# Optimization experiments

Measured on AMD Instinct MI355X. Metric: run time of the kernel, lower is better.

## Reference

```python
import jax, jax.numpy as jnp
import numpy as np

B, D, LC, LQ = 64, 256, 1024, 128
P_DROP = 0.1


def setup_inputs() -> dict:
    key = jax.random.key(0)
    k1, k2, k3 = jax.random.split(key, 3)
    C = jax.random.normal(k1, (B, D, LC), dtype=jnp.float32)
    Q = jax.random.normal(k2, (B, D, LQ), dtype=jnp.float32)
    # xavier_normal_ on [B, 1, 3D]: std = sqrt(2 / (fan_in + fan_out)) = sqrt(2 / (1 + 3D))
    std = (2.0 / (1.0 + 3.0 * D)) ** 0.5
    W = jax.random.normal(k3, (B, 1, 3 * D), dtype=jnp.float32) * std
    return {"C": C, "Q": Q, "W": W}


def reference(C, Q, W):
    # Trilinear similarity, algebraically decomposed:
    # S[b,i,j] = W . cat([Q[:,:,j], C[:,:,i], Q[:,:,j]*C[:,:,i]])
    wq, wc, wm = jnp.split(W[:, 0, :], 3, axis=1)          # each [B, D]
    sq = jnp.einsum('bd,bdj->bj', wq, Q)                    # [B, LQ]
    sc = jnp.einsum('bd,bdi->bi', wc, C)                    # [B, LC]
    sm = jnp.einsum('bd,bdi,bdj->bij', wm, C, Q)            # [B, LC, LQ]
    S = sm + sc[:, :, None] + sq[:, None, :]                # [B, LC, LQ]

    S_ = jax.nn.softmax(S, axis=2)    # row softmax over question positions
    S__ = jax.nn.softmax(S, axis=1)   # column softmax over context positions

    # A = Q @ S_^T : [B, D, LC]
    A = jnp.einsum('bdj,bij->bdi', Q, S_)
    # Bmat = C @ (S_ @ S__^T)^T : first M = S__^T-contracted C, then with S_
    M = jnp.einsum('bdk,bkj->bdj', C, S__)                  # [B, D, LQ]
    Bmat = jnp.einsum('bdj,bij->bdi', M, S_)                # [B, D, LC]

    out = jnp.concatenate([C, A, C * A, C * Bmat], axis=1)  # [B, 4D, LC]

    # F.dropout(p, training=True) with a fixed key (deterministic reference)
    keep = jax.random.bernoulli(jax.random.key(42), 1.0 - P_DROP, out.shape)
    return jnp.where(keep, out / (1.0 - P_DROP), 0.0)
```

## Files before the change

### kernel.cpp

```cpp
#include <hip/hip_runtime.h>
#include <stdint.h>
#include <stddef.h>

#define NB  64
#define ND  256
#define NLC 1024
#define NLQ 128
#define INVKEEP (1.0f/0.9f)

#define OFF_SQP   0u
#define OFF_U     32768u
#define OFF_V     98304u
#define OFF_COLP  106496u
#define OFF_SBT   237568u
#define OFF_QT    4431872u
#define OFF_SBF   8544256u
#define OFF_M     12738560u
#define OFF_QB    13787136u

typedef float f32x4  __attribute__((ext_vector_type(4)));
typedef short bf16x8 __attribute__((ext_vector_type(8)));

__device__ __forceinline__ uint32_t f2bf(float x) {
  const uint32_t u = __float_as_uint(x);
  return (u + 0x7fffu + ((u >> 16) & 1u)) >> 16;
}
__device__ __forceinline__ uint32_t cvtpk(float lo, float hi) {
  uint32_t r;
  asm("v_cvt_pk_bf16_f32 %0, %1, %2" : "=v"(r) : "v"(lo), "v"(hi));
  return r;
}

__device__ __forceinline__ void tf_round(uint32_t& a, uint32_t& b, const int r) {
  a += b;
  b = (b << r) | (b >> (32 - r));
  b ^= a;
}
__device__ __forceinline__ uint32_t threefry_xor(uint32_t x0, uint32_t x1) {
  const uint32_t ks0 = 0u, ks1 = 42u, ks2 = 0x1BD11BDAu ^ 0u ^ 42u;
  x0 += ks0; x1 += ks1;
  tf_round(x0,x1,13); tf_round(x0,x1,15); tf_round(x0,x1,26); tf_round(x0,x1,6);
  x0 += ks1; x1 += ks2 + 1u;
  tf_round(x0,x1,17); tf_round(x0,x1,29); tf_round(x0,x1,16); tf_round(x0,x1,24);
  x0 += ks2; x1 += ks0 + 2u;
  tf_round(x0,x1,13); tf_round(x0,x1,15); tf_round(x0,x1,26); tf_round(x0,x1,6);
  x0 += ks0; x1 += ks1 + 3u;
  tf_round(x0,x1,17); tf_round(x0,x1,29); tf_round(x0,x1,16); tf_round(x0,x1,24);
  x0 += ks1; x1 += ks2 + 4u;
  tf_round(x0,x1,13); tf_round(x0,x1,15); tf_round(x0,x1,26); tf_round(x0,x1,6);
  x0 += ks2; x1 += ks0 + 5u;
  return x0 ^ x1;
}

__global__ __launch_bounds__(256) void k_prep(const float* __restrict__ Q,
                                              const float* __restrict__ W,
                                              float* __restrict__ ws) {
  __shared__ __align__(16) float Qs[64][129];
  __shared__ float wqS[64], wmS[64], wcS[64];
  __shared__ float red[8][128];
  const int n = blockIdx.x;
  const int b = n >> 2, c = n & 3;
  const int d0 = c * 64;
  const int t = threadIdx.x;
  if (t < 64) {
    wqS[t] = W[(size_t)b*768 + d0 + t];
    wcS[t] = W[(size_t)b*768 + 256 + d0 + t];
    wmS[t] = W[(size_t)b*768 + 512 + d0 + t];
  }
  __syncthreads();
  const float* Qb = Q + (size_t)b*ND*NLQ;
  ushort* QBg = (ushort*)(ws + OFF_QB) + (size_t)b*ND*NLQ;
  const int j4 = t & 31, y = t >> 5;
  float sq4[4] = {0.0f, 0.0f, 0.0f, 0.0f};
  #pragma unroll
  for (int p = 0; p < 8; ++p) {
    const int dk = p*8 + y;
    const float4 qv = *(const float4*)&Qb[(size_t)(d0+dk)*NLQ + j4*4];
    *(float4*)&Qs[dk][j4*4] = qv;
    uint2 pk;
    pk.x = cvtpk(qv.x, qv.y);
    pk.y = cvtpk(qv.z, qv.w);
    *(uint2*)&QBg[(size_t)(d0+dk)*NLQ + j4*4] = pk;
    const float wq = wqS[dk];
    sq4[0] = fmaf(wq, qv.x, sq4[0]);
    sq4[1] = fmaf(wq, qv.y, sq4[1]);
    sq4[2] = fmaf(wq, qv.z, sq4[2]);
    sq4[3] = fmaf(wq, qv.w, sq4[3]);
  }
  #pragma unroll
  for (int e = 0; e < 4; ++e) red[y][j4*4 + e] = sq4[e];
  __syncthreads();
  const int j = t >> 1, dh = (t & 1) * 32;
  uint32_t pk16[16];
  #pragma unroll
  for (int kk = 0; kk < 32; kk += 2) {
    const float q0 = fmaf(wmS[dh+kk],   Qs[dh+kk][j],   wcS[dh+kk]);
    const float q1 = fmaf(wmS[dh+kk+1], Qs[dh+kk+1][j], wcS[dh+kk+1]);
    pk16[kk >> 1] = cvtpk(q0, q1);
  }
  ushort* QTg = (ushort*)(ws + OFF_QT) + (size_t)b*NLQ*ND + (size_t)j*ND + d0 + dh;
  *(uint4*)&QTg[0]  = *(uint4*)&pk16[0];
  *(uint4*)&QTg[8]  = *(uint4*)&pk16[4];
  *(uint4*)&QTg[16] = *(uint4*)&pk16[8];
  *(uint4*)&QTg[24] = *(uint4*)&pk16[12];
  if (t < 128) {
    float s = 0.0f;
    #pragma unroll
    for (int yy = 0; yy < 8; ++yy) s += red[yy][t];
    ws[OFF_SQP + ((size_t)b*4 + c)*128 + t] = s;
  }
}

__global__ __launch_bounds__(256) void k_s(const float* __restrict__ C,
                                           float* __restrict__ ws) {
  __shared__ __align__(16) uint8_t smem[37376];
  float  (*Cs)[129] = (float(*)[129])smem;
  ushort (*Qt)[40]  = (ushort(*)[40])(smem + 16512);
  ushort (*T)[128]  = (ushort(*)[128])smem;
  float*  sqS       = (float*)(smem + 32768);
  float  (*colm)[128] = (float(*)[128])(smem + 33280);
  float  (*cols)[128] = (float(*)[128])(smem + 35328);

  const int n  = blockIdx.x;
  const int rr = n & 7, qq = n >> 3;
  const int it = qq & 7;
  const int b  = (qq >> 3) * 8 + rr;
  const int i0 = it * 128;
  const int t  = threadIdx.x;
  if (t < 128) {
    const float* sp = ws + OFF_SQP + (size_t)b*4*128 + t;
    sqS[t] = sp[0] + sp[128] + sp[256] + sp[384];
  }

  const float*  Cb  = C + (size_t)b*ND*NLC;
  const ushort* QTg = (const ushort*)(ws + OFF_QT) + (size_t)b*NLQ*ND;
  const int l  = t & 63, w = t >> 6;
  const int lm = l & 15, lg = l >> 4;

  f32x4 acc[2][8];
  #pragma unroll
  for (int mg = 0; mg < 2; ++mg)
    #pragma unroll
    for (int nf = 0; nf < 8; ++nf) acc[mg][nf] = (f32x4)0.0f;

  for (int d0 = 0; d0 < ND; d0 += 32) {
    __syncthreads();
    #pragma unroll
    for (int p = 0; p < 4; ++p) {
      const int f  = p*256 + t;
      const int dk = f >> 5, x4 = f & 31;
      *(float4*)&Cs[dk][x4*4] = *(const float4*)&Cb[(size_t)(d0+dk)*NLC + i0 + x4*4];
    }
    #pragma unroll
    for (int p = 0; p < 2; ++p) {
      const int f  = p*256 + t;
      const int jr = f >> 2, k8 = (f & 3)*8;
      *(uint4*)&Qt[jr][k8] = *(const uint4*)&QTg[(size_t)jr*ND + d0 + k8];
    }
    __syncthreads();
    bf16x8 bq[8];
    #pragma unroll
    for (int nf = 0; nf < 8; ++nf)
      bq[nf] = *(const bf16x8*)&Qt[nf*16 + lm][lg*8];
    #pragma unroll
    for (int mg = 0; mg < 2; ++mg) {
      const int i = w*32 + mg*16 + lm;
      union { uint32_t u[4]; bf16x8 v; } ca;
      #pragma unroll
      for (int kk = 0; kk < 4; ++kk)
        ca.u[kk] = cvtpk(Cs[lg*8 + kk*2][i], Cs[lg*8 + kk*2 + 1][i]);
      #pragma unroll
      for (int nf = 0; nf < 8; ++nf)
        acc[mg][nf] = __builtin_amdgcn_mfma_f32_16x16x32_bf16(ca.v, bq[nf], acc[mg][nf], 0, 0, 0);
    }
  }

  float sqv[8];
  #pragma unroll
  for (int nf = 0; nf < 8; ++nf) sqv[nf] = sqS[nf*16 + lm];
  __syncthreads();

  #pragma unroll
  for (int mg = 0; mg < 2; ++mg) {
    #pragma unroll
    for (int r = 0; r < 4; ++r) {
      const int row = w*32 + mg*16 + lg*4 + r;
      float sv[8], e[8];
      #pragma unroll
      for (int nf = 0; nf < 8; ++nf) sv[nf] = acc[mg][nf][r] + sqv[nf];
      float mx = sv[0];
      #pragma unroll
      for (int nf = 1; nf < 8; ++nf) mx = fmaxf(mx, sv[nf]);
      mx = fmaxf(mx, __shfl_xor(mx, 1));
      mx = fmaxf(mx, __shfl_xor(mx, 2));
      mx = fmaxf(mx, __shfl_xor(mx, 4));
      mx = fmaxf(mx, __shfl_xor(mx, 8));
      float sm = 0.0f;
      #pragma unroll
      for (int nf = 0; nf < 8; ++nf) { e[nf] = __expf(sv[nf] - mx); sm += e[nf]; }
      sm += __shfl_xor(sm, 1); sm += __shfl_xor(sm, 2);
      sm += __shfl_xor(sm, 4); sm += __shfl_xor(sm, 8);
      const float ir = 1.0f / sm;
      const int po = ((row & 7) ^ ((row >> 3) & 7)) << 3;
      #pragma unroll
      for (int nf = 0; nf < 8; ++nf)
        T[row][(nf*16 + lm) ^ po] = (ushort)f2bf(e[nf] * ir);
      if (lm == 0) ws[OFF_U + (size_t)b*NLC + i0 + row] = __expf(mx) * sm;
    }
  }

  float cmx[8];
  #pragma unroll
  for (int nf = 0; nf < 8; ++nf) {
    float m2 = -3.0e38f;
    #pragma unroll
    for (int mg = 0; mg < 2; ++mg)
      #pragma unroll
      for (int r = 0; r < 4; ++r)
        m2 = fmaxf(m2, acc[mg][nf][r] + sqv[nf]);
    m2 = fmaxf(m2, __shfl_xor(m2, 16));
    m2 = fmaxf(m2, __shfl_xor(m2, 32));
    cmx[nf] = m2;
  }
  if (lg == 0) {
    #pragma unroll
    for (int nf = 0; nf < 8; ++nf) colm[w][nf*16 + lm] = cmx[nf];
  }
  __syncthreads();
  #pragma unroll
  for (int nf = 0; nf < 8; ++nf) {
    const int j = nf*16 + lm;
    const float cmb = fmaxf(fmaxf(colm[0][j], colm[1][j]),
                            fmaxf(colm[2][j], colm[3][j]));
    float cs = 0.0f;
    #pragma unroll
    for (int mg = 0; mg < 2; ++mg)
      #pragma unroll
      for (int r = 0; r < 4; ++r)
        cs += __expf(acc[mg][nf][r] + sqv[nf] - cmb);
    cs += __shfl_xor(cs, 16);
    cs += __shfl_xor(cs, 32);
    if (lg == 0) cols[w][j] = cs;
  }
  __syncthreads();

  ushort* Sb16 = (ushort*)(ws + OFF_SBF) + ((size_t)b*NLC + (size_t)i0)*NLQ;
  #pragma unroll
  for (int p = 0; p < 8; ++p) {
    const int f = p*256 + t;
    const int i = f >> 4, jo = f & 15;
    const int po = ((i & 7) ^ ((i >> 3) & 7)) << 3;
    *(uint4*)&Sb16[(size_t)i*NLQ + jo*8] = *(const uint4*)&T[i][(jo*8) ^ po];
  }
  ushort* SBTg = (ushort*)(ws + OFF_SBT) + (size_t)b*NLQ*NLC + i0;
  #pragma unroll
  for (int p = 0; p < 8; ++p) {
    const int f = p*256 + t;
    const int j = f >> 4, io = f & 15;
    uint32_t wd4[4];
    #pragma unroll
    for (int h = 0; h < 4; ++h) {
      const uint32_t v0 = T[io*8 + h*2    ][j ^ (((h*2    ) ^ (io & 7)) << 3)];
      const uint32_t v1 = T[io*8 + h*2 + 1][j ^ (((h*2 + 1) ^ (io & 7)) << 3)];
      wd4[h] = v0 | (v1 << 16);
    }
    *(uint4*)&SBTg[(size_t)j*NLC + io*8] = *(uint4*)wd4;
  }
  if (t < 128) {
    const float cm = fmaxf(fmaxf(colm[0][t], colm[1][t]),
                           fmaxf(colm[2][t], colm[3][t]));
    const float s  = cols[0][t] + cols[1][t] + cols[2][t] + cols[3][t];
    float2* cp = (float2*)(ws + OFF_COLP) + ((size_t)b*8 + it)*128 + t;
    *cp = make_float2(cm, s);
  }
}

__global__ __launch_bounds__(128) void k_cred(float* __restrict__ ws) {
  const int b = blockIdx.x, j = threadIdx.x;
  const float2* cp = (const float2*)(ws + OFF_COLP) + (size_t)b*8*128 + j;
  float m = -3.0e38f, s = 0.0f;
  #pragma unroll
  for (int it = 0; it < 8; ++it) {
    const float2 p = cp[(size_t)it*128];
    const float nm = fmaxf(m, p.x);
    s = s * __expf(m - nm) + p.y * __expf(p.x - nm);
    m = nm;
  }
  ws[OFF_V + (size_t)b*NLQ + j] = __expf(-m) / s;
}

__global__ __launch_bounds__(256) void k_m(const float* __restrict__ C,
                                           float* __restrict__ ws) {
  __shared__ ushort Cp[32][72];
  __shared__ ushort Ts[128][72];
  __shared__ float u_l[1024];
  __shared__ float v_l[128];
  const int n  = blockIdx.x;
  const int rr = n & 7, qq = n >> 3;
  const int dq = qq & 7;
  const int b  = (qq >> 3) * 8 + rr;
  const int t  = threadIdx.x;
  const int l  = t & 63, w = t >> 6;
  const int wd = w & 1, wj = w >> 1;
  const int lm = l & 15, lg = l >> 4;
  for (int kk = t; kk < 1024; kk += 256) u_l[kk] = ws[OFF_U + (size_t)b*NLC + kk];
  if (t < 128) v_l[t] = ws[OFF_V + (size_t)b*NLQ + t];

  f32x4 acc[4];
  #pragma unroll
  for (int nf = 0; nf < 4; ++nf) acc[nf] = (f32x4)0.0f;

  const float*  Cb   = C + (size_t)b*ND*NLC + (size_t)dq*32*NLC;
  const ushort* SBTg = (const ushort*)(ws + OFF_SBT) + (size_t)b*NLQ*NLC;

  for (int kt = 0; kt < 16; ++kt) {
    const int k0 = kt*64;
    __syncthreads();
    {
      const int dl = t >> 3, kq = t & 7;
      const float4 c0 = *(const float4*)&Cb[(size_t)dl*NLC + k0 + kq*8];
      const float4 c1 = *(const float4*)&Cb[(size_t)dl*NLC + k0 + kq*8 + 4];
      const int kb = k0 + kq*8;
      uint4 pk;
      pk.x = cvtpk(c0.x * u_l[kb+0], c0.y * u_l[kb+1]);
      pk.y = cvtpk(c0.z * u_l[kb+2], c0.w * u_l[kb+3]);
      pk.z = cvtpk(c1.x * u_l[kb+4], c1.y * u_l[kb+5]);
      pk.w = cvtpk(c1.z * u_l[kb+6], c1.w * u_l[kb+7]);
      *(uint4*)&Cp[dl][kq*8] = pk;
    }
    #pragma unroll
    for (int p = 0; p < 4; ++p) {
      const int f = p*256 + t;
      const int jr = f >> 3, k8 = (f & 7)*8;
      *(uint4*)&Ts[jr][k8] = *(const uint4*)&SBTg[(size_t)jr*NLC + k0 + k8];
    }
    __syncthreads();
    #pragma unroll
    for (int ks = 0; ks < 2; ++ks) {
      union { uint32_t u[4]; bf16x8 v; } ca;
      *(uint4*)ca.u = *(const uint4*)&Cp[wd*16 + lm][ks*32 + lg*8];
      #pragma unroll
      for (int nf = 0; nf < 4; ++nf) {
        union { uint32_t u[4]; bf16x8 v; } cb;
        *(uint4*)cb.u = *(const uint4*)&Ts[wj*64 + nf*16 + lm][ks*32 + lg*8];
        acc[nf] = __builtin_amdgcn_mfma_f32_16x16x32_bf16(ca.v, cb.v, acc[nf], 0, 0, 0);
      }
    }
  }
  ushort* Mp = (ushort*)(ws + OFF_M) + (size_t)b*ND*NLQ + (size_t)dq*32*NLQ;
  #pragma unroll
  for (int nf = 0; nf < 4; ++nf) {
    const int j = wj*64 + nf*16 + lm;
    const float vj = v_l[j];
    #pragma unroll
    for (int r = 0; r < 4; ++r) {
      const int d = wd*16 + lg*4 + r;
      Mp[(size_t)d*NLQ + j] = (ushort)f2bf(acc[nf][r] * vj);
    }
  }
}

__global__ __launch_bounds__(256, 4) void k_final(const float* __restrict__ C,
                                                  float* __restrict__ ws,
                                                  float* __restrict__ out) {
  __shared__ __align__(16) uint8_t smem[40960];
  ushort (*St)[128] = (ushort(*)[128])smem;
  ushort (*Qt)[128] = (ushort(*)[128])(smem + 32768);
  ushort (*Mt)[128] = (ushort(*)[128])(smem + 36864);
  float  (*At)[128] = (float (*)[128])smem;
  float  (*Bt)[128] = (float (*)[128])(smem + 8192);

  const int n  = blockIdx.x;
  const int r8 = n & 7, q = n >> 3;
  const int m  = q & 15;
  const int g  = (q >> 4) * 8 + r8;
  const int b  = g & 63;
  const int i0 = (g >> 6) * 128;
  const int d0 = m * 16;
  const int t  = threadIdx.x;

  const ushort* Sp = (const ushort*)(ws + OFF_SBF) + ((size_t)b*NLC + i0)*NLQ;
  #pragma unroll
  for (int p = 0; p < 8; ++p) {
    const int f  = p*256 + t;
    const int jo = f & 15;
    const int il = f >> 4;
    *(uint4*)&St[il][(jo*8) ^ ((il & 7) << 3)] =
        *(const uint4*)&Sp[(size_t)il*NLQ + jo*8];
  }
  const ushort* Qp = (const ushort*)(ws + OFF_QB) + (size_t)b*ND*NLQ + (size_t)d0*NLQ;
  const ushort* Mp = (const ushort*)(ws + OFF_M)  + (size_t)b*ND*NLQ + (size_t)d0*NLQ;
  {
    const int jo = t & 15;
    const int dl = t >> 4;
    const int col = (jo*8) ^ ((dl & 7) << 3);
    *(uint4*)&Qt[dl][col] = *(const uint4*)&Qp[(size_t)dl*NLQ + jo*8];
    *(uint4*)&Mt[dl][col] = *(const uint4*)&Mp[(size_t)dl*NLQ + jo*8];
  }
  __syncthreads();

  const int w  = t >> 6;
  const int l  = t & 63;
  const int lm = l & 15;
  const int lk = (l >> 4) * 8;
  const int sw = (lm & 7) << 3;

  f32x4 accA[2], accB[2];
  #pragma unroll
  for (int f = 0; f < 2; ++f) { accA[f] = (f32x4)0.0f; accB[f] = (f32x4)0.0f; }

  #pragma unroll
  for (int ks = 0; ks < 4; ++ks) {
    const int koff = (ks*32 + lk) ^ sw;
    const bf16x8 qf = *(const bf16x8*)&Qt[lm][koff];
    const bf16x8 mf = *(const bf16x8*)&Mt[lm][koff];
    #pragma unroll
    for (int f = 0; f < 2; ++f) {
      const bf16x8 sf = *(const bf16x8*)&St[(w*2 + f)*16 + lm][koff];
      accA[f] = __builtin_amdgcn_mfma_f32_16x16x32_bf16(qf, sf, accA[f], 0, 0, 0);
      accB[f] = __builtin_amdgcn_mfma_f32_16x16x32_bf16(mf, sf, accB[f], 0, 0, 0);
    }
  }
  __syncthreads();

  const int dwl = (l >> 4) * 4;
  #pragma unroll
  for (int f = 0; f < 2; ++f) {
    const int i = (w*2 + f)*16 + lm;
    #pragma unroll
    for (int r = 0; r < 4; ++r) {
      const int dl = dwl + r;
      const int isw = i ^ ((dl & 7) << 2);
      At[dl][isw] = accA[f][r];
      Bt[dl][isw] = accB[f][r];
    }
  }
  __syncthreads();

  const int il4 = (t & 31) * 4;
  const int dg8 = t >> 5;
  const float* Cb = C + (size_t)b*ND*NLC;
  #pragma unroll 1
  for (int dd = 0; dd < 2; ++dd) {
    const int dl = dd*8 + dg8;
    const int d  = d0 + dl;
    const int isw = il4 ^ ((dl & 7) << 2);
    const float4 a4 = *(const float4*)&At[dl][isw];
    const float4 b4 = *(const float4*)&Bt[dl][isw];
    const float4 c4 = *(const float4*)&Cb[(size_t)d*NLC + i0 + il4];
    const float av[4] = {a4.x, a4.y, a4.z, a4.w};
    const float bv[4] = {b4.x, b4.y, b4.z, b4.w};
    const float cv[4] = {c4.x, c4.y, c4.z, c4.w};
    #pragma unroll
    for (int s = 0; s < 4; ++s) {
      const uint32_t nb = ((((uint32_t)b << 10) + (uint32_t)(s*ND + d)) << 10)
                          + (uint32_t)(i0 + il4);
      float ov[4];
      #pragma unroll
      for (int e = 0; e < 4; ++e) {
        const uint32_t bits = threefry_xor(0u, nb + (uint32_t)e);
        float v;
        if (s == 0)      v = cv[e];
        else if (s == 1) v = av[e];
        else if (s == 2) v = cv[e] * av[e];
        else             v = cv[e] * bv[e];
        ov[e] = (bits < 3865470464u) ? v * INVKEEP : 0.0f;
      }
      *(float4*)&out[nb] = make_float4(ov[0], ov[1], ov[2], ov[3]);
    }
  }
}

extern "C" void kernel_launch(void* const* d_in, const int* in_sizes, int n_in,
                              void* d_out, int out_size, void* d_ws, size_t ws_size,
                              hipStream_t stream) {
  (void)in_sizes; (void)n_in; (void)out_size; (void)ws_size;
  const float* C = (const float*)d_in[0];
  const float* Q = (const float*)d_in[1];
  const float* W = (const float*)d_in[2];
  float* out = (float*)d_out;
  float* ws  = (float*)d_ws;

  hipLaunchKernelGGL(k_prep,  dim3(256),  dim3(256), 0, stream, Q, W, ws);
  hipLaunchKernelGGL(k_s,     dim3(512),  dim3(256), 0, stream, C, ws);
  hipLaunchKernelGGL(k_cred,  dim3(NB),   dim3(128), 0, stream, ws);
  hipLaunchKernelGGL(k_m,     dim3(512),  dim3(256), 0, stream, C, ws);
  hipLaunchKernelGGL(k_final, dim3(8192), dim3(256), 0, stream, C, ws, out);
}
```

Measured before the change: 182.0 us.

## Write final-stage MFMA results directly from registers, load Q/M fragments globally

The final kernel now loads the Q and M bf16 fragments straight from global memory into registers instead of staging them in shared memory. It swaps the MFMA operand order so each lane's accumulator holds consecutive context positions, which lets the epilogue build the dropout output directly from registers. This removes the LDS transpose of the A and B tiles and two barriers. Shared memory drops to the S tile alone, and the occupancy hint rises from 4 to 5 blocks per CU. The cost is narrower per-lane stores (two float4 at a 16-element stride) and uncoalesced per-lane global fragment loads.

Result: slower. 229.1 us (+25.9%).

```diff
diff --git a/kernel.cpp b/kernel.cpp
--- a/kernel.cpp
+++ b/kernel.cpp
@@ -360,15 +360,10 @@
   }
 }
 
-__global__ __launch_bounds__(256, 4) void k_final(const float* __restrict__ C,
+__global__ __launch_bounds__(256, 5) void k_final(const float* __restrict__ C,
                                                   float* __restrict__ ws,
                                                   float* __restrict__ out) {
-  __shared__ __align__(16) uint8_t smem[40960];
-  ushort (*St)[128] = (ushort(*)[128])smem;
-  ushort (*Qt)[128] = (ushort(*)[128])(smem + 32768);
-  ushort (*Mt)[128] = (ushort(*)[128])(smem + 36864);
-  float  (*At)[128] = (float (*)[128])smem;
-  float  (*Bt)[128] = (float (*)[128])(smem + 8192);
+  __shared__ __align__(16) ushort St[128][128];
 
   const int n  = blockIdx.x;
   const int r8 = n & 7, q = n >> 3;
@@ -388,86 +383,64 @@
     *(uint4*)&St[il][(jo*8) ^ ((il & 7) << 3)] =
         *(const uint4*)&Sp[(size_t)il*NLQ + jo*8];
   }
-  const ushort* Qp = (const ushort*)(ws + OFF_QB) + (size_t)b*ND*NLQ + (size_t)d0*NLQ;
-  const ushort* Mp = (const ushort*)(ws + OFF_M)  + (size_t)b*ND*NLQ + (size_t)d0*NLQ;
-  {
-    const int jo = t & 15;
-    const int dl = t >> 4;
-    const int col = (jo*8) ^ ((dl & 7) << 3);
-    *(uint4*)&Qt[dl][col] = *(const uint4*)&Qp[(size_t)dl*NLQ + jo*8];
-    *(uint4*)&Mt[dl][col] = *(const uint4*)&Mp[(size_t)dl*NLQ + jo*8];
-  }
-  __syncthreads();
 
   const int w  = t >> 6;
   const int l  = t & 63;
   const int lm = l & 15;
-  const int lk = (l >> 4) * 8;
+  const int lg = l >> 4;
   const int sw = (lm & 7) << 3;
 
+  const ushort* Qp = (const ushort*)(ws + OFF_QB) + ((size_t)b*ND + d0 + lm)*NLQ;
+  const ushort* Mp = (const ushort*)(ws + OFF_M)  + ((size_t)b*ND + d0 + lm)*NLQ;
+  bf16x8 qf[4], mf[4];
+  #pragma unroll
+  for (int ks = 0; ks < 4; ++ks) {
+    qf[ks] = *(const bf16x8*)&Qp[ks*32 + lg*8];
+    mf[ks] = *(const bf16x8*)&Mp[ks*32 + lg*8];
+  }
+  __syncthreads();
+
   f32x4 accA[2], accB[2];
   #pragma unroll
   for (int f = 0; f < 2; ++f) { accA[f] = (f32x4)0.0f; accB[f] = (f32x4)0.0f; }
 
   #pragma unroll
   for (int ks = 0; ks < 4; ++ks) {
-    const int koff = (ks*32 + lk) ^ sw;
-    const bf16x8 qf = *(const bf16x8*)&Qt[lm][koff];
-    const bf16x8 mf = *(const bf16x8*)&Mt[lm][koff];
+    const int koff = (ks*32 + lg*8) ^ sw;
     #pragma unroll
     for (int f = 0; f < 2; ++f) {
       const bf16x8 sf = *(const bf16x8*)&St[(w*2 + f)*16 + lm][koff];
-      accA[f] = __builtin_amdgcn_mfma_f32_16x16x32_bf16(qf, sf, accA[f], 0, 0, 0);
-      accB[f] = __builtin_amdgcn_mfma_f32_16x16x32_bf16(mf, sf, accB[f], 0, 0, 0);
-    }
-  }
-  __syncthreads();
-
-  const int dwl = (l >> 4) * 4;
-  #pragma unroll
-  for (int f = 0; f < 2; ++f) {
-    const int i = (w*2 + f)*16 + lm;
-    #pragma unroll
-    for (int r = 0; r < 4; ++r) {
-      const int dl = dwl + r;
-      const int isw = i ^ ((dl & 7) << 2);
-      At[dl][isw] = accA[f][r];
-      Bt[dl][isw] = accB[f][r];
-    }
-  }
-  __syncthreads();
-
-  const int il4 = (t & 31) * 4;
-  const int dg8 = t >> 5;
-  const float* Cb = C + (size_t)b*ND*NLC;
+      accA[f] = __builtin_amdgcn_mfma_f32_16x16x32_bf16(sf, qf[ks], accA[f], 0, 0, 0);
+      accB[f] = __builtin_amdgcn_mfma_f32_16x16x32_bf16(sf, mf[ks], accB[f], 0, 0, 0);
+    }
+  }
+
+  const int d  = d0 + lm;
+  const int ib = i0 + w*32 + lg*4;
+  const float* Crow = C + ((size_t)b*ND + d)*NLC;
+  const float4 c0 = *(const float4*)&Crow[ib];
+  const float4 c1 = *(const float4*)&Crow[ib + 16];
+  const float cv0[4] = {c0.x, c0.y, c0.z, c0.w};
+  const float cv1[4] = {c1.x, c1.y, c1.z, c1.w};
   #pragma unroll 1
-  for (int dd = 0; dd < 2; ++dd) {
-    const int dl = dd*8 + dg8;
-    const int d  = d0 + dl;
-    const int isw = il4 ^ ((dl & 7) << 2);
-    const float4 a4 = *(const float4*)&At[dl][isw];
-    const float4 b4 = *(const float4*)&Bt[dl][isw];
-    const float4 c4 = *(const float4*)&Cb[(size_t)d*NLC + i0 + il4];
-    const float av[4] = {a4.x, a4.y, a4.z, a4.w};
-    const float bv[4] = {b4.x, b4.y, b4.z, b4.w};
-    const float cv[4] = {c4.x, c4.y, c4.z, c4.w};
-    #pragma unroll
-    for (int s = 0; s < 4; ++s) {
-      const uint32_t nb = ((((uint32_t)b << 10) + (uint32_t)(s*ND + d)) << 10)
-                          + (uint32_t)(i0 + il4);
-      float ov[4];
-      #pragma unroll
-      for (int e = 0; e < 4; ++e) {
-        const uint32_t bits = threefry_xor(0u, nb + (uint32_t)e);
-        float v;
-        if (s == 0)      v = cv[e];
-        else if (s == 1) v = av[e];
-        else if (s == 2) v = cv[e] * av[e];
-        else             v = cv[e] * bv[e];
-        ov[e] = (bits < 3865470464u) ? v * INVKEEP : 0.0f;
-      }
-      *(float4*)&out[nb] = make_float4(ov[0], ov[1], ov[2], ov[3]);
-    }
+  for (int s = 0; s < 4; ++s) {
+    const uint32_t nb0 = ((((uint32_t)b << 10) + (uint32_t)(s*ND + d)) << 10)
+                         + (uint32_t)ib;
+    float o0[4], o1[4];
+    #pragma unroll
+    for (int e = 0; e < 4; ++e) {
+      const uint32_t bits0 = threefry_xor(0u, nb0 + (uint32_t)e);
+      const uint32_t bits1 = threefry_xor(0u, nb0 + 16u + (uint32_t)e);
+      float va, vb;
+      if (s == 0)      { va = cv0[e];             vb = cv1[e]; }
+      else if (s == 1) { va = accA[0][e];         vb = accA[1][e]; }
+      else if (s == 2) { va = cv0[e]*accA[0][e];  vb = cv1[e]*accA[1][e]; }
+      else             { va = cv0[e]*accB[0][e];  vb = cv1[e]*accB[1][e]; }
+      o0[e] = (bits0 < 3865470464u) ? va * INVKEEP : 0.0f;
+      o1[e] = (bits1 < 3865470464u) ? vb * INVKEEP : 0.0f;
+    }
+    *(float4*)&out[nb0]       = make_float4(o0[0], o0[1], o0[2], o0[3]);
+    *(float4*)&out[nb0 + 16]  = make_float4(o1[0], o1[1], o1[2], o1[3]);
   }
 }
 
```
